# Kernel tuning notes

Hardware: AMD Instinct MI355X
Metric: run time of the kernel (lower is better)

## Reference

```python
import jax, jax.numpy as jnp
import numpy as np

EMBED_DIM = 2048
NUM_HEADS = 16
HEAD_DIM = EMBED_DIM // NUM_HEADS
ROPE_BASE = 10000.0


def _rope_cos_sin(seq_len, head_dim, dtype):
    # half-split (LLaMA-style) rotary embedding tables, shape [S, D]
    inv_freq = 1.0 / (ROPE_BASE ** (jnp.arange(0, head_dim, 2, dtype=jnp.float32) / head_dim))
    ang = jnp.arange(seq_len, dtype=jnp.float32)[:, None] * inv_freq[None, :]  # [S, D/2]
    cos = jnp.concatenate([jnp.cos(ang), jnp.cos(ang)], axis=-1).astype(dtype)
    sin = jnp.concatenate([jnp.sin(ang), jnp.sin(ang)], axis=-1).astype(dtype)
    return cos, sin


def _rotate_half(t):
    d = t.shape[-1] // 2
    return jnp.concatenate([-t[..., d:], t[..., :d]], axis=-1)


def setup_inputs() -> dict:
    key = jax.random.key(0)
    ks = jax.random.split(key, 9)
    B, S, E = 2, 2048, EMBED_DIM
    sc = 1.0 / np.sqrt(E)
    return {
        "x": jax.random.normal(ks[0], (B, S, E), jnp.float32),
        "Wq": jax.random.normal(ks[1], (E, E), jnp.float32) * sc,
        "bq": jax.random.normal(ks[2], (E,), jnp.float32) * 0.01,
        "Wk": jax.random.normal(ks[3], (E, E), jnp.float32) * sc,
        "bk": jax.random.normal(ks[4], (E,), jnp.float32) * 0.01,
        "Wv": jax.random.normal(ks[5], (E, E), jnp.float32) * sc,
        "bv": jax.random.normal(ks[6], (E,), jnp.float32) * 0.01,
        "Wo": jax.random.normal(ks[7], (E, E), jnp.float32) * sc,
        "bo": jax.random.normal(ks[8], (E,), jnp.float32) * 0.01,
    }


def reference(x, Wq, bq, Wk, bk, Wv, bv, Wo, bo):
    B, S, E = x.shape
    H, D = NUM_HEADS, HEAD_DIM

    def split_heads(t):  # [B,S,E] -> [B,H,S,D]
        return t.reshape(B, S, H, D).transpose(0, 2, 1, 3)

    # torch nn.Linear: y = x @ W^T + b
    q = split_heads(x @ Wq.T + bq)
    k = split_heads(x @ Wk.T + bk)
    v = split_heads(x @ Wv.T + bv)

    cos, sin = _rope_cos_sin(S, D, x.dtype)  # [S, D]
    q = q * cos + _rotate_half(q) * sin
    k = k * cos + _rotate_half(k) * sin

    scale = 1.0 / jnp.sqrt(jnp.asarray(D, x.dtype))
    scores = jnp.einsum("bhsd,bhtd->bhst", q, k) * scale  # [B,H,S,S]
    attn = jax.nn.softmax(scores, axis=-1)
    ctx = jnp.einsum("bhst,bhtd->bhsd", attn, v)  # [B,H,S,D]
    ctx = ctx.transpose(0, 2, 1, 3).reshape(B, S, E)
    return ctx @ Wo.T + bo
```

## Files before the change

kernel.cpp:

```cpp
#include <hip/hip_runtime.h>
#include <stdint.h>

typedef unsigned short u16;
typedef unsigned int u32;
typedef __bf16 bf16x8 __attribute__((ext_vector_type(8)));
typedef float f32x4 __attribute__((ext_vector_type(4)));
typedef float f32x16 __attribute__((ext_vector_type(16)));

#define NB 2
#define NS 2048
#define NE 2048
#define NH 16
#define ND 128
#define NM (NB*NS)

__device__ __forceinline__ float bf2f(u16 u){
  union { unsigned u; float f; } v; v.u = ((unsigned)u) << 16; return v.f;
}
__device__ __forceinline__ u16 f2bf(float f){
  union { float f; unsigned u; } v; v.f = f;
  unsigned r = v.u + 0x7fffu + ((v.u >> 16) & 1u);
  return (u16)(r >> 16);
}
__device__ __forceinline__ void gl_lds16(const u16* g, u16* l){
  __builtin_amdgcn_global_load_lds((const __attribute__((address_space(1))) unsigned int*)g,
                                   (__attribute__((address_space(3))) unsigned int*)l, 16, 0, 0);
}

__global__ __launch_bounds__(256) void k_cvt(const float* __restrict__ in, u16* __restrict__ out, int n4){
  int i = blockIdx.x * 256 + threadIdx.x;
  int stride = gridDim.x * 256;
  for (; i < n4; i += stride){
    float4 v = ((const float4*)in)[i];
    ushort4 o;
    o.x = f2bf(v.x); o.y = f2bf(v.y); o.z = f2bf(v.z); o.w = f2bf(v.w);
    ((ushort4*)out)[i] = o;
  }
}

__global__ __launch_bounds__(256) void k_cvt4(const float* __restrict__ w0, const float* __restrict__ w1,
                                              const float* __restrict__ w2, const float* __restrict__ w3,
                                              u16* __restrict__ o0, u16* __restrict__ o1,
                                              u16* __restrict__ o2, u16* __restrict__ o3){
  const int n4 = NE * NE / 4;
  int i = blockIdx.x * 256 + threadIdx.x;
  int stride = gridDim.x * 256;
  for (; i < 4 * n4; i += stride){
    int seg = i >> 20;
    int off = i & (n4 - 1);
    const float* in = seg == 0 ? w0 : seg == 1 ? w1 : seg == 2 ? w2 : w3;
    u16*        out = seg == 0 ? o0 : seg == 1 ? o1 : seg == 2 ? o2 : o3;
    float4 v = ((const float4*)in)[off];
    ushort4 o;
    o.x = f2bf(v.x); o.y = f2bf(v.y); o.z = f2bf(v.z); o.w = f2bf(v.w);
    ((ushort4*)out)[off] = o;
  }
}

__global__ __launch_bounds__(256) void k_tables(float* __restrict__ cosT, float* __restrict__ sinT){
  int idx = blockIdx.x * 256 + threadIdx.x;
  int s = idx >> 6, i = idx & 63;
  float inv = exp2f(-(float)(2 * i) * (13.287712379549449f / 128.0f));
  float ang = (float)s * inv;
  float c = cosf(ang), sn = sinf(ang);
  cosT[s * ND + i]      = c;  cosT[s * ND + 64 + i] = c;
  sinT[s * ND + i]      = sn; sinT[s * ND + 64 + i] = sn;
}

template<int MODE>
__global__ __launch_bounds__(512, 2) void k_gemm(const u16* __restrict__ A, const u16* __restrict__ W,
                                                 const float* __restrict__ bias,
                                                 const float* __restrict__ cosT, const float* __restrict__ sinT,
                                                 float qs, void* __restrict__ outp)
{
  __shared__ __align__(16) u16 lds[49152];
  const int t    = threadIdx.x;
  const int lane = t & 63;
  const int g    = lane >> 4;
  const int q    = lane & 15;
  const int wid  = t >> 6;
  const int wr   = (wid >> 1) * 64;
  const int wc   = (wid & 1) * 64;

  const int bid = blockIdx.x;
  const int v   = (bid & 7) * 32 + (bid >> 3);
  const int bm  = (v >> 4) * 256;
  const int bn  = (v & 15) * 128;

  int aoff[4], aldso[4], boff[2], bldso[2];
  #pragma unroll
  for (int c = 0; c < 4; ++c){
    int o = c * 8192 + t * 16;
    int row = o >> 7;
    int cb = (o & 127) ^ ((row & 7) << 4);
    aldso[c] = o >> 1;
    aoff[c]  = row * NE + (cb >> 1);
  }
  #pragma unroll
  for (int c = 0; c < 2; ++c){
    int o = c * 8192 + t * 16;
    int row = o >> 7;
    int cb = (o & 127) ^ ((row & 7) << 4);
    bldso[c] = o >> 1;
    boff[c]  = row * NE + (cb >> 1);
  }
  const u16* Abase = A + (size_t)bm * NE;
  const u16* Wbase = W + (size_t)bn * NE;

  int ard[2][4], brd[2][4];
  #pragma unroll
  for (int kk = 0; kk < 2; ++kk){
    #pragma unroll
    for (int m = 0; m < 4; ++m){
      int row = wr + m * 16 + q;
      ard[kk][m] = row * 128 + ((kk * 64 + g * 16) ^ ((row & 7) << 4));
    }
    #pragma unroll
    for (int n = 0; n < 4; ++n){
      int row = wc + n * 16 + q;
      brd[kk][n] = row * 128 + ((kk * 64 + g * 16) ^ ((row & 7) << 4));
    }
  }

  #pragma unroll
  for (int c = 0; c < 4; ++c) gl_lds16(Abase + aoff[c], lds + aldso[c]);
  #pragma unroll
  for (int c = 0; c < 2; ++c) gl_lds16(Wbase + boff[c], lds + 16384 + bldso[c]);

  f32x4 acc[4][4] = {};

  for (int kt = 0; kt < 32; ++kt){
    const int cbb = (kt & 1) ? 24576 : 0;
    if (kt < 31){
      const int sbb = cbb ^ 24576;
      const int go  = (kt + 1) * 64;
      #pragma unroll
      for (int c = 0; c < 4; ++c) gl_lds16(Abase + go + aoff[c], lds + sbb + aldso[c]);
      #pragma unroll
      for (int c = 0; c < 2; ++c) gl_lds16(Wbase + go + boff[c], lds + sbb + 16384 + bldso[c]);
      asm volatile("s_waitcnt vmcnt(6)" ::: "memory");
    } else {
      asm volatile("s_waitcnt vmcnt(0)" ::: "memory");
    }
    __builtin_amdgcn_s_barrier();

    const char* Ap = (const char*)(lds + cbb);
    const char* Bp = (const char*)(lds + cbb + 16384);

    {
      bf16x8 af[4], bfr[4];
      #pragma unroll
      for (int m = 0; m < 4; ++m) af[m]  = *(const bf16x8*)(Ap + ard[0][m]);
      #pragma unroll
      for (int n = 0; n < 4; ++n) bfr[n] = *(const bf16x8*)(Bp + brd[0][n]);
      __builtin_amdgcn_s_setprio(1);
      #pragma unroll
      for (int m = 0; m < 4; ++m)
        #pragma unroll
        for (int n = 0; n < 4; ++n)
          acc[m][n] = __builtin_amdgcn_mfma_f32_16x16x32_bf16(af[m], bfr[n], acc[m][n], 0, 0, 0);
      __builtin_amdgcn_s_setprio(0);
    }
    __builtin_amdgcn_s_barrier();

    {
      bf16x8 af[4], bfr[4];
      #pragma unroll
      for (int m = 0; m < 4; ++m) af[m]  = *(const bf16x8*)(Ap + ard[1][m]);
      #pragma unroll
      for (int n = 0; n < 4; ++n) bfr[n] = *(const bf16x8*)(Bp + brd[1][n]);
      __builtin_amdgcn_s_setprio(1);
      #pragma unroll
      for (int m = 0; m < 4; ++m)
        #pragma unroll
        for (int n = 0; n < 4; ++n)
          acc[m][n] = __builtin_amdgcn_mfma_f32_16x16x32_bf16(af[m], bfr[n], acc[m][n], 0, 0, 0);
      __builtin_amdgcn_s_setprio(0);
    }
    __builtin_amdgcn_s_barrier();
  }

  if constexpr (MODE == 2){
    float* out = (float*)outp;
    #pragma unroll
    for (int m = 0; m < 4; ++m)
      #pragma unroll
      for (int n = 0; n < 4; ++n){
        int col = bn + wc + n * 16 + q;
        float bv = bias[col];
        #pragma unroll
        for (int j = 0; j < 4; ++j){
          int row = bm + wr + m * 16 + g * 4 + j;
          out[(size_t)row * NE + col] = acc[m][n][j] + bv;
        }
      }
  } else if constexpr (MODE == 1){
    u16* out = (u16*)outp;
    #pragma unroll
    for (int m = 0; m < 4; ++m)
      #pragma unroll
      for (int n = 0; n < 4; ++n){
        int col = bn + wc + n * 16 + q;
        int h = col >> 7, d = col & 127;
        float bv = bias[col];
        #pragma unroll
        for (int j = 0; j < 4; ++j){
          int row = bm + wr + m * 16 + g * 4 + j;
          int b = row >> 11, s = row & 2047;
          out[(((size_t)(b * NH + h)) * NS + s) * ND + d] = f2bf(acc[m][n][j] + bv);
        }
      }
  } else {
    u16* out = (u16*)outp;
    #pragma unroll
    for (int m = 0; m < 4; ++m)
      #pragma unroll
      for (int n = 0; n < 4; ++n){
        int cl = wc + n * 16 + q;
        float bv = bias[bn + cl];
        #pragma unroll
        for (int j = 0; j < 4; ++j){
          int rl = wr + m * 16 + g * 4 + j;
          lds[rl * 132 + cl] = f2bf(acc[m][n][j] + bv);
        }
      }
    __syncthreads();
    #pragma unroll
    for (int m = 0; m < 4; ++m)
      #pragma unroll
      for (int n = 0; n < 4; ++n){
        int cl  = wc + n * 16 + q;
        int col = bn + cl;
        int h = col >> 7;
        float bv = bias[col];
        #pragma unroll
        for (int j = 0; j < 4; ++j){
          int rl = wr + m * 16 + g * 4 + j;
          int row = bm + rl;
          int b = row >> 11, s = row & 2047;
          float mine    = acc[m][n][j] + bv;
          float partner = bf2f(lds[rl * 132 + (cl ^ 64)]);
          float rot = (cl < 64) ? -partner : partner;
          float val = (mine * cosT[s * ND + cl] + rot * sinT[s * ND + cl]) * qs;
          out[(((size_t)(b * NH + h)) * NS + s) * ND + cl] = f2bf(val);
        }
      }
  }
}

__global__ __launch_bounds__(256) void k_tr(const u16* __restrict__ Va, u16* __restrict__ Vt){
  __shared__ u16 tile[32][33];
  int d0 = blockIdx.x * 32, s0 = blockIdx.y * 32, bh = blockIdx.z;
  int tx = threadIdx.x & 31, ty = threadIdx.x >> 5;
  #pragma unroll
  for (int r = 0; r < 4; ++r)
    tile[ty + 8 * r][tx] = Va[((size_t)bh * NS + s0 + ty + 8 * r) * ND + d0 + tx];
  __syncthreads();
  #pragma unroll
  for (int r = 0; r < 4; ++r)
    Vt[((size_t)bh * ND + d0 + ty + 8 * r) * NS + s0 + tx] = tile[tx][ty + 8 * r];
}

template<bool D1>
__device__ __forceinline__ void pswap(u32 &a, u32 &b){
  if constexpr (D1) asm volatile("v_permlane32_swap_b32 %0, %1" : "+v"(a), "+v"(b));
  else              asm volatile("v_permlane32_swap_b32 %0, %1" : "+v"(b), "+v"(a));
}

#define AT_BODY(KT, SCC, SCN, KSTG, VSTG, KNXT, VCUR, SK, SV, VM, LAST)               \
  {                                                                                   \
    if (SK){ const int kb = ((KT) + 2) * 64 * ND;                                     \
      _Pragma("unroll") for (int c = 0; c < 4; ++c)                                   \
        gl_lds16(Kbase + kb + koff[c], (KSTG) + kldso[c]); }                          \
    if (SV){ const int vb = ((KT) + 1) * 64;                                          \
      _Pragma("unroll") for (int c = 0; c < 4; ++c)                                   \
        gl_lds16(Vbase + vb + voff[c], (VSTG) + vldso[c]); }                          \
    asm volatile("s_waitcnt vmcnt(" VM ")" ::: "memory");                             \
    __builtin_amdgcn_s_barrier();                                                     \
    float tA[8];                                                                      \
    _Pragma("unroll") for (int i = 0; i < 8; ++i)                                     \
      tA[i] = fmaxf(fmaxf(SCC[0][2*i], SCC[0][2*i+1]), fmaxf(SCC[1][2*i], SCC[1][2*i+1])); \
    float pmax = fmaxf(fmaxf(fmaxf(tA[0],tA[1]), fmaxf(tA[2],tA[3])),                 \
                       fmaxf(fmaxf(tA[4],tA[5]), fmaxf(tA[6],tA[7])));                \
    if (!(LAST)){                                                                     \
      SCN[0] = (f32x16)(0.f); SCN[1] = (f32x16)(0.f);                                 \
      __builtin_amdgcn_s_setprio(1);                                                  \
      _Pragma("unroll") for (int kk = 0; kk < 8; ++kk){                               \
        bf16x8 kf = *(const bf16x8*)((KNXT) + krd[0][kk]);                            \
        SCN[0] = __builtin_amdgcn_mfma_f32_32x32x16_bf16(kf, qf[kk], SCN[0], 0, 0, 0);\
      }                                                                               \
      __builtin_amdgcn_s_setprio(0);                                                  \
    }                                                                                 \
    pmax = fmaxf(pmax, __shfl_xor(pmax, 32));                                         \
    if (__any(pmax > mrow + 8.0f)){                                                   \
      float nm = fmaxf(mrow, pmax);                                                   \
      float rs = exp2f(mrow - nm);                                                    \
      lrow *= rs;                                                                     \
      _Pragma("unroll") for (int dt = 0; dt < 4; ++dt)                                \
        _Pragma("unroll") for (int r = 0; r < 16; ++r) acc[dt][r] *= rs;              \
      mrow = nm;                                                                      \
    }                                                                                 \
    float ts = 0.f;                                                                   \
    _Pragma("unroll") for (int r = 0; r < 16; ++r){                                   \
      float e = exp2f(SCC[0][r] - mrow); SCC[0][r] = e; ts += e; }                    \
    if (!(LAST)){                                                                     \
      __builtin_amdgcn_s_setprio(1);                                                  \
      _Pragma("unroll") for (int kk = 0; kk < 8; ++kk){                               \
        bf16x8 kf = *(const bf16x8*)((KNXT) + krd[1][kk]);                            \
        SCN[1] = __builtin_amdgcn_mfma_f32_32x32x16_bf16(kf, qf[kk], SCN[1], 0, 0, 0);\
      }                                                                               \
      __builtin_amdgcn_s_setprio(0);                                                  \
    }                                                                                 \
    _Pragma("unroll") for (int r = 0; r < 16; ++r){                                   \
      float e = exp2f(SCC[1][r] - mrow); SCC[1][r] = e; ts += e; }                    \
    ts += __shfl_xor(ts, 32);                                                         \
    lrow += ts;                                                                       \
    __builtin_amdgcn_s_setprio(1);                                                    \
    _Pragma("unroll") for (int t2 = 0; t2 < 2; ++t2)                                  \
      _Pragma("unroll") for (int kk2 = 0; kk2 < 2; ++kk2){                            \
        u32 a0, a1, b0, b1;                                                           \
        asm("v_cvt_pk_bf16_f32 %0, %1, %2" : "=v"(a0) : "v"(SCC[t2][8*kk2+0]), "v"(SCC[t2][8*kk2+1])); \
        asm("v_cvt_pk_bf16_f32 %0, %1, %2" : "=v"(a1) : "v"(SCC[t2][8*kk2+2]), "v"(SCC[t2][8*kk2+3])); \
        asm("v_cvt_pk_bf16_f32 %0, %1, %2" : "=v"(b0) : "v"(SCC[t2][8*kk2+4]), "v"(SCC[t2][8*kk2+5])); \
        asm("v_cvt_pk_bf16_f32 %0, %1, %2" : "=v"(b1) : "v"(SCC[t2][8*kk2+6]), "v"(SCC[t2][8*kk2+7])); \
        pswap<D1>(a0, b0); pswap<D1>(a1, b1);                                         \
        union { u32 u[4]; bf16x8 v; } pf;                                             \
        pf.u[0] = a0; pf.u[1] = a1; pf.u[2] = b0; pf.u[3] = b1;                       \
        const int kkf = 2*t2 + kk2;                                                   \
        _Pragma("unroll") for (int dt = 0; dt < 4; ++dt){                             \
          bf16x8 vf = *(const bf16x8*)((VCUR) + vrd[kkf][dt]);                        \
          acc[dt] = __builtin_amdgcn_mfma_f32_32x32x16_bf16(vf, pf.v, acc[dt], 0, 0, 0); \
        }                                                                             \
      }                                                                               \
    __builtin_amdgcn_s_setprio(0);                                                    \
    if (!(LAST)) __builtin_amdgcn_s_barrier();                                        \
  }

template<bool D1>
__device__ __forceinline__ void attn_impl(const u16* __restrict__ Qa, const u16* __restrict__ Ka,
                                          const u16* __restrict__ Vt, u16* __restrict__ ctx,
                                          u16* Ks0, u16* Ks1, u16* Vs0, u16* Vs1)
{
  const int t    = threadIdx.x;
  const int lane = t & 63;
  const int w    = t >> 6;
  const int l31  = lane & 31;
  const int hi   = lane >> 5;

  const int v   = (blockIdx.x & 7) * 64 + (blockIdx.x >> 3);
  const int qb  = v & 15;
  const int bh  = v >> 4;
  const int q0  = qb * 128 + w * 32;

  int koff[4], kldso[4], voff[4], vldso[4];
  #pragma unroll
  for (int c = 0; c < 4; ++c){
    int o = c * 4096 + t * 16;
    { int row = o >> 8, col = o & 255; int cs = col ^ ((row & 15) << 4);
      kldso[c] = o >> 1;  koff[c] = row * ND + (cs >> 1); }
    { int row = o >> 7, col = o & 127; int cs = col ^ ((row & 7) << 4);
      vldso[c] = o >> 1;  voff[c] = row * NS + (cs >> 1); }
  }
  const u16* Kbase = Ka + (size_t)bh * NS * ND;
  const u16* Vbase = Vt + (size_t)bh * ND * NS;

  bf16x8 qf[8];
  #pragma unroll
  for (int kk = 0; kk < 8; ++kk)
    qf[kk] = *(const bf16x8*)(Qa + ((size_t)bh * NS + q0 + l31) * ND + kk * 16 + hi * 8);

  #pragma unroll
  for (int c = 0; c < 4; ++c) gl_lds16(Kbase + koff[c], Ks0 + kldso[c]);
  #pragma unroll
  for (int c = 0; c < 4; ++c) gl_lds16(Vbase + voff[c], Vs0 + vldso[c]);
  #pragma unroll
  for (int c = 0; c < 4; ++c) gl_lds16(Kbase + 64 * ND + koff[c], Ks1 + kldso[c]);

  int krd[2][8], vrd[4][4];
  #pragma unroll
  for (int t2 = 0; t2 < 2; ++t2){
    const int row = t2 * 32 + l31, sw = (row & 15) << 4;
    #pragma unroll
    for (int kk = 0; kk < 8; ++kk)
      krd[t2][kk] = row * 256 + ((kk * 32 + hi * 16) ^ sw);
  }
  #pragma unroll
  for (int dt = 0; dt < 4; ++dt){
    const int row = dt * 32 + l31, sw = (row & 7) << 4;
    #pragma unroll
    for (int kk = 0; kk < 4; ++kk)
      vrd[kk][dt] = row * 128 + ((kk * 32 + hi * 16) ^ sw);
  }

  asm volatile("s_waitcnt vmcnt(8)" ::: "memory");
  __builtin_amdgcn_s_barrier();

  f32x16 scA[2], scB[2];
  scA[0] = (f32x16)(0.f); scA[1] = (f32x16)(0.f);
  {
    const char* Kl = (const char*)Ks0;
    #pragma unroll
    for (int t2 = 0; t2 < 2; ++t2)
      #pragma unroll
      for (int kk = 0; kk < 8; ++kk){
        bf16x8 kf = *(const bf16x8*)(Kl + krd[t2][kk]);
        scA[t2] = __builtin_amdgcn_mfma_f32_32x32x16_bf16(kf, qf[kk], scA[t2], 0, 0, 0);
      }
  }
  __builtin_amdgcn_s_barrier();

  f32x16 acc[4] = {};
  float mrow = -3e38f, lrow = 0.f;

  for (int kt = 0; kt < 30; kt += 2){
    AT_BODY(kt,     scA, scB, Ks0, Vs1, (const char*)Ks1, (const char*)Vs0, 1, 1, "8", 0);
    AT_BODY(kt + 1, scB, scA, Ks1, Vs0, (const char*)Ks0, (const char*)Vs1, 1, 1, "8", 0);
  }
  AT_BODY(30, scA, scB, Ks0, Vs1, (const char*)Ks1, (const char*)Vs0, 0, 1, "4", 0);
  AT_BODY(31, scB, scA, Ks1, Vs0, (const char*)Ks0, (const char*)Vs1, 0, 0, "0", 1);

  const float inv = 1.0f / lrow;
  const int b = bh >> 4, h = bh & 15;
  const int s = q0 + l31;
  #pragma unroll
  for (int dt = 0; dt < 4; ++dt)
    #pragma unroll
    for (int a2 = 0; a2 < 4; ++a2){
      const int d0 = dt * 32 + 8 * a2 + 4 * hi;
      ushort4 o;
      o.x = f2bf(acc[dt][4*a2+0] * inv);
      o.y = f2bf(acc[dt][4*a2+1] * inv);
      o.z = f2bf(acc[dt][4*a2+2] * inv);
      o.w = f2bf(acc[dt][4*a2+3] * inv);
      *(ushort4*)(ctx + ((size_t)(b * NS + s)) * NE + h * ND + d0) = o;
    }
}

__global__ __launch_bounds__(256, 2) void k_attn(const u16* __restrict__ Qa, const u16* __restrict__ Ka,
                                                 const u16* __restrict__ Vt, u16* __restrict__ ctx)
{
  __shared__ __align__(16) u16 Ks[2][64 * 128];
  __shared__ __align__(16) u16 Vs[2][128 * 64];
  const int lane = threadIdx.x & 63;
  u32 xx = (u32)lane, yy = 64u + (u32)lane;
  asm volatile("v_permlane32_swap_b32 %0, %1" : "+v"(xx), "+v"(yy));
  const bool isD1 = (xx == (u32)(lane < 32 ? lane : lane + 32));
  if (isD1) attn_impl<true >(Qa, Ka, Vt, ctx, &Ks[0][0], &Ks[1][0], &Vs[0][0], &Vs[1][0]);
  else      attn_impl<false>(Qa, Ka, Vt, ctx, &Ks[0][0], &Ks[1][0], &Vs[0][0], &Vs[1][0]);
}

extern "C" void kernel_launch(void* const* d_in, const int* in_sizes, int n_in,
                              void* d_out, int out_size, void* d_ws, size_t ws_size,
                              hipStream_t stream)
{
  const float* x  = (const float*)d_in[0];
  const float* Wq = (const float*)d_in[1];
  const float* bq = (const float*)d_in[2];
  const float* Wk = (const float*)d_in[3];
  const float* bk = (const float*)d_in[4];
  const float* Wv = (const float*)d_in[5];
  const float* bv = (const float*)d_in[6];
  const float* Wo = (const float*)d_in[7];
  const float* bo = (const float*)d_in[8];

  char* ws = (char*)d_ws;
  u16*   xbf  = (u16*)(ws);
  u16*   wqb  = (u16*)(ws + 16777216);
  u16*   wkb  = (u16*)(ws + 25165824);
  u16*   wvb  = (u16*)(ws + 33554432);
  u16*   wob  = (u16*)(ws + 41943040);
  float* cosT = (float*)(ws + 50331648);
  float* sinT = (float*)(ws + 51380224);
  u16*   Qa   = (u16*)(ws + 52428800);
  u16*   Ka   = (u16*)(ws + 69206016);
  u16*   Va   = (u16*)(ws + 85983232);
  u16*   Vt   = xbf;
  u16*   ctx  = Va;

  const float sl = 0.08838834764831845f * 1.4426950408889634f;

  k_cvt<<<1024, 256, 0, stream>>>(x, xbf, NM * NE / 4);
  k_cvt4<<<2048, 256, 0, stream>>>(Wq, Wk, Wv, Wo, wqb, wkb, wvb, wob);
  k_tables<<<NS * 64 / 256, 256, 0, stream>>>(cosT, sinT);

  k_gemm<0><<<256, 512, 0, stream>>>(xbf, wqb, bq, cosT, sinT, sl,   (void*)Qa);
  k_gemm<0><<<256, 512, 0, stream>>>(xbf, wkb, bk, cosT, sinT, 1.0f, (void*)Ka);
  k_gemm<1><<<256, 512, 0, stream>>>(xbf, wvb, bv, nullptr, nullptr, 1.0f, (void*)Va);

  k_tr<<<dim3(ND / 32, NS / 32, NB * NH), 256, 0, stream>>>(Va, Vt);

  k_attn<<<512, 256, 0, stream>>>(Qa, Ka, Vt, ctx);

  k_gemm<2><<<256, 512, 0, stream>>>(ctx, wob, bo, nullptr, nullptr, 1.0f, d_out);
}
```

Baseline: 284.0 us.

## Use 4-wave GEMM with larger per-wave tiles and fuse V transpose into epilogue

The GEMM drops from 8 waves to 4 waves per block, so each wave now computes a 128x64 tile with 8x4 MFMA accumulators. The two K-substeps are merged into one loop with a single barrier per substep. The V projection epilogue now transposes through LDS and writes V^T directly with vector stores, which removes the separate transpose kernel and its extra pass over global memory. The cost is higher register pressure and fewer waves per CU to hide latency, and the workspace buffer aliasing is rearranged (ctx now reuses xbf).

Measured after the change: 366.1 us. 1.29x slower.

```diff
diff --git a/kernel.cpp b/kernel.cpp
--- a/kernel.cpp
+++ b/kernel.cpp
@@ -4,6 +4,7 @@
 typedef unsigned short u16;
 typedef unsigned int u32;
 typedef __bf16 bf16x8 __attribute__((ext_vector_type(8)));
+typedef u16 u16x8 __attribute__((ext_vector_type(8)));
 typedef float f32x4 __attribute__((ext_vector_type(4)));
 typedef float f32x16 __attribute__((ext_vector_type(16)));
 
@@ -68,7 +69,7 @@
 }
 
 template<int MODE>
-__global__ __launch_bounds__(512, 2) void k_gemm(const u16* __restrict__ A, const u16* __restrict__ W,
+__global__ __launch_bounds__(256, 1) void k_gemm(const u16* __restrict__ A, const u16* __restrict__ W,
                                                  const float* __restrict__ bias,
                                                  const float* __restrict__ cosT, const float* __restrict__ sinT,
                                                  float qs, void* __restrict__ outp)
@@ -79,7 +80,7 @@
   const int g    = lane >> 4;
   const int q    = lane & 15;
   const int wid  = t >> 6;
-  const int wr   = (wid >> 1) * 64;
+  const int wr   = (wid >> 1) * 128;
   const int wc   = (wid & 1) * 64;
 
   const int bid = blockIdx.x;
@@ -87,47 +88,24 @@
   const int bm  = (v >> 4) * 256;
   const int bn  = (v & 15) * 128;
 
-  int aoff[4], aldso[4], boff[2], bldso[2];
-  #pragma unroll
-  for (int c = 0; c < 4; ++c){
-    int o = c * 8192 + t * 16;
-    int row = o >> 7;
-    int cb = (o & 127) ^ ((row & 7) << 4);
-    aldso[c] = o >> 1;
-    aoff[c]  = row * NE + (cb >> 1);
-  }
-  #pragma unroll
-  for (int c = 0; c < 2; ++c){
-    int o = c * 8192 + t * 16;
-    int row = o >> 7;
-    int cb = (o & 127) ^ ((row & 7) << 4);
-    bldso[c] = o >> 1;
-    boff[c]  = row * NE + (cb >> 1);
-  }
-  const u16* Abase = A + (size_t)bm * NE;
-  const u16* Wbase = W + (size_t)bn * NE;
-
-  int ard[2][4], brd[2][4];
-  #pragma unroll
-  for (int kk = 0; kk < 2; ++kk){
-    #pragma unroll
-    for (int m = 0; m < 4; ++m){
-      int row = wr + m * 16 + q;
-      ard[kk][m] = row * 128 + ((kk * 64 + g * 16) ^ ((row & 7) << 4));
-    }
-    #pragma unroll
-    for (int n = 0; n < 4; ++n){
-      int row = wc + n * 16 + q;
-      brd[kk][n] = row * 128 + ((kk * 64 + g * 16) ^ ((row & 7) << 4));
-    }
-  }
-
-  #pragma unroll
-  for (int c = 0; c < 4; ++c) gl_lds16(Abase + aoff[c], lds + aldso[c]);
-  #pragma unroll
-  for (int c = 0; c < 2; ++c) gl_lds16(Wbase + boff[c], lds + 16384 + bldso[c]);
-
-  f32x4 acc[4][4] = {};
+  const int srow   = t >> 3;
+  const int scb    = ((t * 16) & 127) ^ ((srow & 7) << 4);
+  const int aldso0 = t * 8;
+  const u16* Abase = A + (size_t)bm * NE + srow * NE + (scb >> 1);
+  const u16* Wbase = W + (size_t)bn * NE + srow * NE + (scb >> 1);
+
+  int xo[2];
+  xo[0] = (g * 16)      ^ ((q & 7) << 4);
+  xo[1] = (64 + g * 16) ^ ((q & 7) << 4);
+  const int arow = (wr + q) * 128;
+  const int brow = (wc + q) * 128;
+
+  #pragma unroll
+  for (int c = 0; c < 8; ++c) gl_lds16(Abase + c * (32 * NE), lds + c * 2048 + aldso0);
+  #pragma unroll
+  for (int c = 0; c < 4; ++c) gl_lds16(Wbase + c * (32 * NE), lds + 16384 + c * 2048 + aldso0);
+
+  f32x4 acc[8][4] = {};
 
   for (int kt = 0; kt < 32; ++kt){
     const int cbb = (kt & 1) ? 24576 : 0;
@@ -135,104 +113,100 @@
       const int sbb = cbb ^ 24576;
       const int go  = (kt + 1) * 64;
       #pragma unroll
-      for (int c = 0; c < 4; ++c) gl_lds16(Abase + go + aoff[c], lds + sbb + aldso[c]);
-      #pragma unroll
-      for (int c = 0; c < 2; ++c) gl_lds16(Wbase + go + boff[c], lds + sbb + 16384 + bldso[c]);
-      asm volatile("s_waitcnt vmcnt(6)" ::: "memory");
+      for (int c = 0; c < 8; ++c) gl_lds16(Abase + go + c * (32 * NE), lds + sbb + c * 2048 + aldso0);
+      #pragma unroll
+      for (int c = 0; c < 4; ++c) gl_lds16(Wbase + go + c * (32 * NE), lds + sbb + 16384 + c * 2048 + aldso0);
+      asm volatile("s_waitcnt vmcnt(12)" ::: "memory");
     } else {
       asm volatile("s_waitcnt vmcnt(0)" ::: "memory");
     }
     __builtin_amdgcn_s_barrier();
 
-    const char* Ap = (const char*)(lds + cbb);
-    const char* Bp = (const char*)(lds + cbb + 16384);
-
-    {
-      bf16x8 af[4], bfr[4];
-      #pragma unroll
-      for (int m = 0; m < 4; ++m) af[m]  = *(const bf16x8*)(Ap + ard[0][m]);
-      #pragma unroll
-      for (int n = 0; n < 4; ++n) bfr[n] = *(const bf16x8*)(Bp + brd[0][n]);
+    const char* Ap = (const char*)(lds) + cbb * 2;
+    const char* Bp = (const char*)(lds) + cbb * 2 + 32768;
+    #pragma unroll
+    for (int kk = 0; kk < 2; ++kk){
+      bf16x8 af[8], bfr[4];
+      #pragma unroll
+      for (int m = 0; m < 8; ++m) af[m]  = *(const bf16x8*)(Ap + arow + m * 2048 + xo[kk]);
+      #pragma unroll
+      for (int n = 0; n < 4; ++n) bfr[n] = *(const bf16x8*)(Bp + brow + n * 2048 + xo[kk]);
       __builtin_amdgcn_s_setprio(1);
       #pragma unroll
-      for (int m = 0; m < 4; ++m)
+      for (int m = 0; m < 8; ++m)
         #pragma unroll
         for (int n = 0; n < 4; ++n)
           acc[m][n] = __builtin_amdgcn_mfma_f32_16x16x32_bf16(af[m], bfr[n], acc[m][n], 0, 0, 0);
       __builtin_amdgcn_s_setprio(0);
     }
     __builtin_amdgcn_s_barrier();
-
-    {
-      bf16x8 af[4], bfr[4];
-      #pragma unroll
-      for (int m = 0; m < 4; ++m) af[m]  = *(const bf16x8*)(Ap + ard[1][m]);
-      #pragma unroll
-      for (int n = 0; n < 4; ++n) bfr[n] = *(const bf16x8*)(Bp + brd[1][n]);
-      __builtin_amdgcn_s_setprio(1);
-      #pragma unroll
-      for (int m = 0; m < 4; ++m)
-        #pragma unroll
-        for (int n = 0; n < 4; ++n)
-          acc[m][n] = __builtin_amdgcn_mfma_f32_16x16x32_bf16(af[m], bfr[n], acc[m][n], 0, 0, 0);
-      __builtin_amdgcn_s_setprio(0);
-    }
-    __builtin_amdgcn_s_barrier();
   }
 
   if constexpr (MODE == 2){
     float* out = (float*)outp;
     #pragma unroll
-    for (int m = 0; m < 4; ++m)
-      #pragma unroll
-      for (int n = 0; n < 4; ++n){
-        int col = bn + wc + n * 16 + q;
-        float bv = bias[col];
+    for (int n = 0; n < 4; ++n){
+      int col = bn + wc + n * 16 + q;
+      float bv = bias[col];
+      #pragma unroll
+      for (int m = 0; m < 8; ++m)
         #pragma unroll
         for (int j = 0; j < 4; ++j){
           int row = bm + wr + m * 16 + g * 4 + j;
           out[(size_t)row * NE + col] = acc[m][n][j] + bv;
         }
-      }
+    }
   } else if constexpr (MODE == 1){
     u16* out = (u16*)outp;
-    #pragma unroll
-    for (int m = 0; m < 4; ++m)
-      #pragma unroll
-      for (int n = 0; n < 4; ++n){
-        int col = bn + wc + n * 16 + q;
-        int h = col >> 7, d = col & 127;
-        float bv = bias[col];
+    __syncthreads();
+    #pragma unroll
+    for (int n = 0; n < 4; ++n){
+      int d = wc + n * 16 + q;
+      float bv = bias[bn + d];
+      #pragma unroll
+      for (int m = 0; m < 8; ++m)
         #pragma unroll
         for (int j = 0; j < 4; ++j){
-          int row = bm + wr + m * 16 + g * 4 + j;
-          int b = row >> 11, s = row & 2047;
-          out[(((size_t)(b * NH + h)) * NS + s) * ND + d] = f2bf(acc[m][n][j] + bv);
+          int sl = wr + m * 16 + g * 4 + j;
+          lds[d * 264 + sl] = f2bf(acc[m][n][j] + bv);
         }
-      }
+    }
+    __syncthreads();
+    const int b = bm >> 11, h = bn >> 7, sbase = bm & 2047;
+    const int dq = t >> 4;
+    const int sq = (t & 15) * 16;
+    #pragma unroll
+    for (int rep = 0; rep < 8; ++rep){
+      int d = rep * 16 + dq;
+      const u16* src = lds + d * 264 + sq;
+      u16* dp = out + ((size_t)((b * NH + h) * ND + d)) * NS + sbase + sq;
+      *(u16x8*)(dp)     = *(const u16x8*)(src);
+      *(u16x8*)(dp + 8) = *(const u16x8*)(src + 8);
+    }
   } else {
     u16* out = (u16*)outp;
-    #pragma unroll
-    for (int m = 0; m < 4; ++m)
-      #pragma unroll
-      for (int n = 0; n < 4; ++n){
-        int cl = wc + n * 16 + q;
-        float bv = bias[bn + cl];
+    __syncthreads();
+    #pragma unroll
+    for (int n = 0; n < 4; ++n){
+      int cl = wc + n * 16 + q;
+      float bv = bias[bn + cl];
+      #pragma unroll
+      for (int m = 0; m < 8; ++m)
         #pragma unroll
         for (int j = 0; j < 4; ++j){
           int rl = wr + m * 16 + g * 4 + j;
           lds[rl * 132 + cl] = f2bf(acc[m][n][j] + bv);
         }
-      }
+    }
     __syncthreads();
     #pragma unroll
-    for (int m = 0; m < 4; ++m)
-      #pragma unroll
-      for (int n = 0; n < 4; ++n){
-        int cl  = wc + n * 16 + q;
-        int col = bn + cl;
-        int h = col >> 7;
-        float bv = bias[col];
+    for (int n = 0; n < 4; ++n){
+      int cl  = wc + n * 16 + q;
+      int col = bn + cl;
+      int h = col >> 7;
+      float bv = bias[col];
+      #pragma unroll
+      for (int m = 0; m < 8; ++m)
         #pragma unroll
         for (int j = 0; j < 4; ++j){
           int rl = wr + m * 16 + g * 4 + j;
@@ -244,21 +218,8 @@
           float val = (mine * cosT[s * ND + cl] + rot * sinT[s * ND + cl]) * qs;
           out[(((size_t)(b * NH + h)) * NS + s) * ND + cl] = f2bf(val);
         }
-      }
-  }
-}
-
-__global__ __launch_bounds__(256) void k_tr(const u16* __restrict__ Va, u16* __restrict__ Vt){
-  __shared__ u16 tile[32][33];
-  int d0 = blockIdx.x * 32, s0 = blockIdx.y * 32, bh = blockIdx.z;
-  int tx = threadIdx.x & 31, ty = threadIdx.x >> 5;
-  #pragma unroll
-  for (int r = 0; r < 4; ++r)
-    tile[ty + 8 * r][tx] = Va[((size_t)bh * NS + s0 + ty + 8 * r) * ND + d0 + tx];
-  __syncthreads();
-  #pragma unroll
-  for (int r = 0; r < 4; ++r)
-    Vt[((size_t)bh * ND + d0 + ty + 8 * r) * NS + s0 + tx] = tile[tx][ty + 8 * r];
+    }
+  }
 }
 
 template<bool D1>
@@ -473,9 +434,8 @@
   float* sinT = (float*)(ws + 51380224);
   u16*   Qa   = (u16*)(ws + 52428800);
   u16*   Ka   = (u16*)(ws + 69206016);
-  u16*   Va   = (u16*)(ws + 85983232);
-  u16*   Vt   = xbf;
-  u16*   ctx  = Va;
+  u16*   Vt   = (u16*)(ws + 85983232);
+  u16*   ctx  = xbf;
 
   const float sl = 0.08838834764831845f * 1.4426950408889634f;
 
@@ -483,13 +443,11 @@
   k_cvt4<<<2048, 256, 0, stream>>>(Wq, Wk, Wv, Wo, wqb, wkb, wvb, wob);
   k_tables<<<NS * 64 / 256, 256, 0, stream>>>(cosT, sinT);
 
-  k_gemm<0><<<256, 512, 0, stream>>>(xbf, wqb, bq, cosT, sinT, sl,   (void*)Qa);
-  k_gemm<0><<<256, 512, 0, stream>>>(xbf, wkb, bk, cosT, sinT, 1.0f, (void*)Ka);
-  k_gemm<1><<<256, 512, 0, stream>>>(xbf, wvb, bv, nullptr, nullptr, 1.0f, (void*)Va);
-
-  k_tr<<<dim3(ND / 32, NS / 32, NB * NH), 256, 0, stream>>>(Va, Vt);
+  k_gemm<0><<<256, 256, 0, stream>>>(xbf, wqb, bq, cosT, sinT, sl,   (void*)Qa);
+  k_gemm<0><<<256, 256, 0, stream>>>(xbf, wkb, bk, cosT, sinT, 1.0f, (void*)Ka);
+  k_gemm<1><<<256, 256, 0, stream>>>(xbf, wvb, bv, nullptr, nullptr, 1.0f, (void*)Vt);
 
   k_attn<<<512, 256, 0, stream>>>(Qa, Ka, Vt, ctx);
 
-  k_gemm<2><<<256, 512, 0, stream>>>(ctx, wob, bo, nullptr, nullptr, 1.0f, d_out);
-}
+  k_gemm<2><<<256, 256, 0, stream>>>(ctx, wob, bo, nullptr, nullptr, 1.0f, d_out);
+}
```
